# Kernel tuning notes

Hardware: AMD Instinct MI355X
Metric: run time of the kernel (lower is better)

## Reference

```python
import jax, jax.numpy as jnp
import numpy as np

EPS = 1e-5
N_NODES = 100000
N_EDGES = 1600000
IN_F, HID_F, OUT_F = 128, 128, 64


def setup_inputs() -> dict:
    key = jax.random.key(0)
    ks = jax.random.split(key, 8)
    def xavier(k, fan_in, fan_out):
        lim = float(np.sqrt(6.0 / (fan_in + fan_out)))
        return jax.random.uniform(k, (fan_in, fan_out), jnp.float32, -lim, lim)
    return {
        "features": jax.random.normal(ks[0], (N_NODES, IN_F), jnp.float32),
        "src": jax.random.randint(ks[1], (N_EDGES,), 0, N_NODES, jnp.int64 if jax.config.jax_enable_x64 else jnp.int32),
        "dst": jax.random.randint(ks[2], (N_EDGES,), 0, N_NODES, jnp.int64 if jax.config.jax_enable_x64 else jnp.int32),
        "W_self1": xavier(ks[3], IN_F, HID_F),
        "W_neigh1": xavier(ks[4], IN_F, HID_F),
        "b1": jnp.zeros((HID_F,), jnp.float32),
        "gamma1": jnp.ones((HID_F,), jnp.float32),
        "beta1": jnp.zeros((HID_F,), jnp.float32),
        "W_self2": xavier(ks[5], HID_F, OUT_F),
        "W_neigh2": xavier(ks[6], HID_F, OUT_F),
        "b2": jnp.zeros((OUT_F,), jnp.float32),
        "gamma2": jnp.ones((OUT_F,), jnp.float32),
        "beta2": jnp.zeros((OUT_F,), jnp.float32),
    }


def _sage_conv(h, src, dst, W_self, W_neigh, b, n_nodes):
    # mean aggregation of source-node features onto destination nodes
    agg = jax.ops.segment_sum(h[src], dst, num_segments=n_nodes)   # [N, d]
    deg = jax.ops.segment_sum(jnp.ones_like(dst, dtype=h.dtype), dst, num_segments=n_nodes)
    h_neigh = agg / jnp.maximum(deg, 1.0)[:, None]                  # zero-degree -> 0
    return h @ W_self + h_neigh @ W_neigh + b


def _batchnorm(h, gamma, beta):
    # training-mode BatchNorm1d: batch stats over node dim, biased variance
    mu = jnp.mean(h, axis=0)
    var = jnp.mean(jnp.square(h - mu), axis=0)
    return (h - mu) * jax.lax.rsqrt(var + EPS) * gamma + beta


def reference(features, src, dst, W_self1, W_neigh1, b1, gamma1, beta1,
              W_self2, W_neigh2, b2, gamma2, beta2):
    n = features.shape[0]
    h = _sage_conv(features, src, dst, W_self1, W_neigh1, b1, n)
    h = jax.nn.relu(_batchnorm(h, gamma1, beta1))
    h = _sage_conv(h, src, dst, W_self2, W_neigh2, b2, n)
    return _batchnorm(h, gamma2, beta2)
```

## Files before the change

### kernel.cpp

```cpp
#include <hip/hip_runtime.h>

#define EPS_BN 1e-5f
#define BINSHIFT 9
#define BINW 512
#define P_EPB 8192
#define LDS_CAP 10240
#define NREP 32

typedef __attribute__((ext_vector_type(8))) short short8;
typedef __attribute__((ext_vector_type(4))) float f32x4;

__device__ __forceinline__ unsigned short f2bf(float x) {
    unsigned int u = __float_as_uint(x);
    u += 0x7fffu + ((u >> 16) & 1u);
    return (unsigned short)(u >> 16);
}
__device__ __forceinline__ float bf2f(unsigned short h) {
    return __uint_as_float(((unsigned int)h) << 16);
}
__device__ __forceinline__ float bflo(unsigned u) { return __uint_as_float(u << 16); }
__device__ __forceinline__ float bfhi(unsigned u) { return __uint_as_float(u & 0xffff0000u); }

__device__ __forceinline__ void scan512(int* a, int t) {
    for (int off = 1; off < 512; off <<= 1) {
        int v = (t >= off) ? a[t - off] : 0;
        __syncthreads();
        a[t] += v;
        __syncthreads();
    }
}
__device__ __forceinline__ void scan256(int* a, int t) {
    for (int off = 1; off < 256; off <<= 1) {
        int v = (t >= off) ? a[t - off] : 0;
        __syncthreads();
        a[t] += v;
        __syncthreads();
    }
}

__global__ __launch_bounds__(256) void prep_kernel(
    const float* __restrict__ Ws1, const float* __restrict__ Wn1,
    const float* __restrict__ Ws2, const float* __restrict__ Wn2,
    unsigned short* __restrict__ W1f, unsigned short* __restrict__ W2f,
    const int* __restrict__ dst, int* __restrict__ counts, int E, int NB, int wB) {
    int tid = threadIdx.x;
    if (blockIdx.x < wB) {
        int i = blockIdx.x * 256 + tid;
        if (i < 128 * 256) {
            int j = i & 7, L = (i >> 3) & 63, c = (i >> 9) & 15, kk = i >> 13;
            int k = kk * 32 + (L >> 4) * 8 + j;
            int col = c * 16 + (L & 15);
            float v = (col < 128) ? Ws1[k * 128 + col] : Wn1[k * 128 + (col - 128)];
            W1f[i] = f2bf(v);
        } else {
            int idx = i - 128 * 256;
            if (idx < 128 * 128) {
                int j = idx & 7, L = (idx >> 3) & 63, c = (idx >> 9) & 7, kk = idx >> 12;
                int k = kk * 32 + (L >> 4) * 8 + j;
                int col = c * 16 + (L & 15);
                float v = (col < 64) ? Ws2[k * 64 + col] : Wn2[k * 64 + (col - 64)];
                W2f[idx] = f2bf(v);
            }
        }
    } else {
        __shared__ int hist[512];
        int blk = blockIdx.x - wB;
        int e0 = blk * P_EPB, e1 = min(e0 + P_EPB, E);
        for (int b = tid; b < 512; b += 256) hist[b] = 0;
        __syncthreads();
        for (int e = e0 + tid; e < e1; e += 256) atomicAdd(&hist[dst[e] >> BINSHIFT], 1);
        __syncthreads();
        for (int b = tid; b < NB; b += 256) counts[blk * NB + b] = hist[b];
    }
}

__global__ __launch_bounds__(256) void p2a(const int* __restrict__ counts,
                                           int* __restrict__ segrel,
                                           int* __restrict__ tot, int NB, int NBLK) {
    __shared__ int s[256];
    int b = blockIdx.x, t = threadIdx.x;
    int v = (t < NBLK) ? counts[t * NB + b] : 0;
    s[t] = v;
    __syncthreads();
    scan256(s, t);
    if (t < NBLK) segrel[t * NB + b] = s[t] - v;
    if (t == 255) tot[b] = s[255];
}

__global__ __launch_bounds__(512) void p3_scatter(const int* __restrict__ src,
                                                  const int* __restrict__ dst,
                                                  const int* __restrict__ segrel,
                                                  const int* __restrict__ tot,
                                                  unsigned* __restrict__ epack,
                                                  int E, int NB) {
    __shared__ unsigned lp[P_EPB];
    __shared__ int hist[512];
    __shared__ int sBase[513];
    __shared__ int cursor[512];
    __shared__ int bbase[512];
    int t = threadIdx.x;
    int blk = blockIdx.x;
    int e0 = blk * P_EPB, e1 = min(e0 + P_EPB, E), m = e1 - e0;
    int tv = (t < NB) ? tot[t] : 0;
    bbase[t] = tv;
    __syncthreads();
    scan512(bbase, t);
    bbase[t] -= tv;
    hist[t] = 0;
    __syncthreads();
    for (int e = e0 + t; e < e1; e += 512) atomicAdd(&hist[dst[e] >> BINSHIFT], 1);
    __syncthreads();
    int h = hist[t];
    scan512(hist, t);
    int excl = hist[t] - h;
    sBase[t] = excl;
    cursor[t] = excl;
    if (t == 0) sBase[512] = m;
    __syncthreads();
    for (int e = e0 + t; e < e1; e += 512) {
        int d = dst[e];
        int pos = atomicAdd(&cursor[d >> BINSHIFT], 1);
        lp[pos] = ((unsigned)src[e] << BINSHIFT) | ((unsigned)d & (BINW - 1));
    }
    __syncthreads();
    for (int i = t; i < m; i += 512) {
        int lo = 0, hi = NB;
        while (hi - lo > 1) {
            int mid = (lo + hi) >> 1;
            if (sBase[mid] <= i) lo = mid; else hi = mid;
        }
        epack[bbase[lo] + segrel[blk * NB + lo] + (i - sBase[lo])] = lp[i];
    }
}

__global__ __launch_bounds__(512) void p4_csr(const unsigned* __restrict__ epack,
                                              const int* __restrict__ tot,
                                              int* __restrict__ row_start,
                                              int* __restrict__ cntg,
                                              float* __restrict__ inv_deg,
                                              int* __restrict__ csr_src, int N, int NB) {
    __shared__ int ncnt[512];
    __shared__ int cursor[512];
    __shared__ int bb[512];
    __shared__ int lsrc[LDS_CAP];
    int t = threadIdx.x;
    int b = blockIdx.x;
    int tv = (t < NB) ? tot[t] : 0;
    bb[t] = tv;
    __syncthreads();
    scan512(bb, t);
    int e1 = bb[b];
    int e0 = bb[b] - tot[b];
    int m = e1 - e0;
    int nbase = b << BINSHIFT;
    int nn = min(N - nbase, BINW);
    ncnt[t] = 0;
    __syncthreads();
    for (int i = e0 + t; i < e1; i += 512)
        atomicAdd(&ncnt[epack[i] & (BINW - 1)], 1);
    __syncthreads();
    int c = ncnt[t];
    scan512(ncnt, t);
    int excl = ncnt[t] - c;
    if (t < nn) {
        int node = nbase + t;
        row_start[node] = e0 + excl;
        cntg[node] = c;
        inv_deg[node] = 1.0f / fmaxf((float)c, 1.0f);
    }
    cursor[t] = excl;
    __syncthreads();
    for (int i = e0 + t; i < e1; i += 512) {
        unsigned v = epack[i];
        int pos = atomicAdd(&cursor[v & (BINW - 1)], 1);
        if (pos < LDS_CAP) lsrc[pos] = (int)(v >> BINSHIFT);
    }
    __syncthreads();
    int mm = min(m, LDS_CAP);
    for (int i = t; i < mm; i += 512) csr_src[e0 + i] = lsrc[i];
}

template <int MT, int MSELF, bool SELFBF, bool FUSEBN, bool AFP32>
__global__ __launch_bounds__(256) void gemm_dual(const unsigned short* __restrict__ Ab,
                                                 const float* __restrict__ Af,
                                                 const unsigned short* __restrict__ Wf,
                                                 float* __restrict__ YselfF,
                                                 unsigned short* __restrict__ YselfB,
                                                 unsigned short* __restrict__ Ynb, int N,
                                                 const float* __restrict__ sums,
                                                 const float* __restrict__ gamma,
                                                 const float* __restrict__ beta,
                                                 float invN) {
    constexpr int K = 128;
    constexpr int NCT = MT / 16;
    constexpr int KS = K / 32;
    constexpr int MNB = MT - MSELF;
    __shared__ unsigned short Bl[KS * NCT * 64 * 8];
    __shared__ float ssc[128], ssh[128];

    for (int i = threadIdx.x; i < KS * NCT * 64; i += 256)
        ((short8*)Bl)[i] = ((const short8*)Wf)[i];
    if (FUSEBN && threadIdx.x < 128) {
        int c = threadIdx.x;
        float su = 0.f, sq = 0.f;
        for (int r = 0; r < NREP; r++) {
            su += sums[r * 256 + c];
            sq += sums[r * 256 + 128 + c];
        }
        float mu = su * invN;
        float var = sq * invN - mu * mu;
        float sc = gamma[c] * rsqrtf(var + EPS_BN);
        ssc[c] = sc;
        ssh[c] = beta[c] - mu * sc;
    }
    __syncthreads();

    int wv = threadIdx.x >> 6, lane = threadIdx.x & 63;
    int row0 = blockIdx.x * 128 + wv * 32;
    int m = lane & 15, quad = lane >> 4;

    short8 afrag[2][KS];
#pragma unroll
    for (int t = 0; t < 2; t++) {
        int arow = row0 + t * 16 + m;
        if (arow >= N) arow = N - 1;
#pragma unroll
        for (int kk = 0; kk < KS; kk++) {
            short8 raw;
            if (AFP32) {
                const float* ap = Af + (size_t)arow * K + quad * 8 + kk * 32;
                f32x4 a = *(const f32x4*)ap;
                f32x4 b = *(const f32x4*)(ap + 4);
#pragma unroll
                for (int j = 0; j < 4; j++) {
                    raw[j] = (short)f2bf(a[j]);
                    raw[4 + j] = (short)f2bf(b[j]);
                }
            } else {
                raw = *(const short8*)(Ab + (size_t)arow * K + quad * 8 + kk * 32);
            }
            if (FUSEBN) {
#pragma unroll
                for (int j = 0; j < 8; j++) {
                    int c = kk * 32 + quad * 8 + j;
                    float f = bf2f((unsigned short)raw[j]) * ssc[c] + ssh[c];
                    raw[j] = (short)f2bf(fmaxf(f, 0.f));
                }
            }
            afrag[t][kk] = raw;
        }
    }

    f32x4 acc[2][NCT];
#pragma unroll
    for (int t = 0; t < 2; t++)
        for (int c = 0; c < NCT; c++)
            for (int j = 0; j < 4; j++) acc[t][c][j] = 0.f;

#pragma unroll
    for (int kk = 0; kk < KS; kk++) {
#pragma unroll
        for (int c = 0; c < NCT; c++) {
            short8 bfrag = *(const short8*)&Bl[((kk * NCT + c) * 64 + lane) * 8];
#pragma unroll
            for (int t = 0; t < 2; t++)
                acc[t][c] = __builtin_amdgcn_mfma_f32_16x16x32_bf16(afrag[t][kk], bfrag,
                                                                    acc[t][c], 0, 0, 0);
        }
    }

#pragma unroll
    for (int t = 0; t < 2; t++) {
#pragma unroll
        for (int c = 0; c < NCT; c++) {
            int colg = c * 16 + m;
#pragma unroll
            for (int r = 0; r < 4; r++) {
                int row = row0 + t * 16 + quad * 4 + r;
                if (row < N) {
                    float v = acc[t][c][r];
                    if (colg < MSELF) {
                        if (SELFBF)
                            YselfB[(size_t)row * MSELF + colg] = f2bf(v);
                        else
                            YselfF[(size_t)row * MSELF + colg] = v;
                    } else {
                        Ynb[(size_t)row * MNB + (colg - MSELF)] = f2bf(v);
                    }
                }
            }
        }
    }
}

__global__ __launch_bounds__(256) void agg_row128(const unsigned int* __restrict__ Sb,
                                                  const unsigned int* __restrict__ T,
                                                  const int* __restrict__ row_start,
                                                  const int* __restrict__ cnt,
                                                  const float* __restrict__ inv_deg,
                                                  const int* __restrict__ csr_src,
                                                  const float* __restrict__ bias,
                                                  unsigned int* __restrict__ Out,
                                                  float* __restrict__ sums,
                                                  int N, int totalWaves) {
    int wv = threadIdx.x >> 6, lane = threadIdx.x & 63;
    int c = lane * 2;
    float bs0 = bias[c], bs1 = bias[c + 1];
    float S0 = 0.f, S1 = 0.f, Q0 = 0.f, Q1 = 0.f;
    for (int n = blockIdx.x * 4 + wv; n < N; n += totalWaves) {
        int start = row_start[n];
        int ec = cnt[n];
        float inv = inv_deg[n];
        float a0 = 0.f, a1 = 0.f;
        int e = 0;
        for (; e + 7 < ec; e += 8) {
            int i0 = csr_src[start + e];
            int i1 = csr_src[start + e + 1];
            int i2 = csr_src[start + e + 2];
            int i3 = csr_src[start + e + 3];
            int i4 = csr_src[start + e + 4];
            int i5 = csr_src[start + e + 5];
            int i6 = csr_src[start + e + 6];
            int i7 = csr_src[start + e + 7];
            unsigned u0 = T[(size_t)i0 * 64 + lane];
            unsigned u1 = T[(size_t)i1 * 64 + lane];
            unsigned u2 = T[(size_t)i2 * 64 + lane];
            unsigned u3 = T[(size_t)i3 * 64 + lane];
            unsigned u4 = T[(size_t)i4 * 64 + lane];
            unsigned u5 = T[(size_t)i5 * 64 + lane];
            unsigned u6 = T[(size_t)i6 * 64 + lane];
            unsigned u7 = T[(size_t)i7 * 64 + lane];
            a0 += bflo(u0) + bflo(u1) + bflo(u2) + bflo(u3) +
                  bflo(u4) + bflo(u5) + bflo(u6) + bflo(u7);
            a1 += bfhi(u0) + bfhi(u1) + bfhi(u2) + bfhi(u3) +
                  bfhi(u4) + bfhi(u5) + bfhi(u6) + bfhi(u7);
        }
        for (; e < ec; e++) {
            unsigned u0 = T[(size_t)csr_src[start + e] * 64 + lane];
            a0 += bflo(u0);
            a1 += bfhi(u0);
        }
        unsigned su = Sb[(size_t)n * 64 + lane];
        float h0 = bflo(su) + a0 * inv + bs0;
        float h1 = bfhi(su) + a1 * inv + bs1;
        Out[(size_t)n * 64 + lane] = (unsigned)f2bf(h0) | ((unsigned)f2bf(h1) << 16);
        S0 += h0; Q0 += h0 * h0;
        S1 += h1; Q1 += h1 * h1;
    }
    __shared__ float ls[256];
    ls[threadIdx.x] = 0.f;
    __syncthreads();
    atomicAdd(&ls[c], S0);
    atomicAdd(&ls[c + 1], S1);
    atomicAdd(&ls[128 + c], Q0);
    atomicAdd(&ls[129 + c], Q1);
    __syncthreads();
    float* dstS = sums + (size_t)(blockIdx.x & (NREP - 1)) * 256;
    atomicAdd(&dstS[threadIdx.x], ls[threadIdx.x]);
}

__global__ __launch_bounds__(256) void agg_row64(const unsigned int* __restrict__ T,
                                                 const int* __restrict__ row_start,
                                                 const int* __restrict__ cnt,
                                                 const float* __restrict__ inv_deg,
                                                 const int* __restrict__ csr_src,
                                                 const float* __restrict__ bias,
                                                 float* Self, float* __restrict__ sums,
                                                 int N, int totalHalf) {
    int wv = threadIdx.x >> 6, L = threadIdx.x & 63;
    int g = L >> 5, h = L & 31;
    int c = h * 2;
    float bs0 = bias[c], bs1 = bias[c + 1];
    float S0 = 0.f, S1 = 0.f, Q0 = 0.f, Q1 = 0.f;
    for (int n = (blockIdx.x * 4 + wv) * 2 + g; n < N; n += totalHalf) {
        int start = row_start[n];
        int ec = cnt[n];
        float inv = inv_deg[n];
        float a0 = 0.f, a1 = 0.f;
        int e = 0;
        for (; e + 3 < ec; e += 4) {
            int i0 = csr_src[start + e];
            int i1 = csr_src[start + e + 1];
            int i2 = csr_src[start + e + 2];
            int i3 = csr_src[start + e + 3];
            unsigned u0 = T[(size_t)i0 * 32 + h];
            unsigned u1 = T[(size_t)i1 * 32 + h];
            unsigned u2 = T[(size_t)i2 * 32 + h];
            unsigned u3 = T[(size_t)i3 * 32 + h];
            a0 += bflo(u0) + bflo(u1) + bflo(u2) + bflo(u3);
            a1 += bfhi(u0) + bfhi(u1) + bfhi(u2) + bfhi(u3);
        }
        for (; e < ec; e++) {
            unsigned u0 = T[(size_t)csr_src[start + e] * 32 + h];
            a0 += bflo(u0);
            a1 += bfhi(u0);
        }
        size_t off = (size_t)n * 64 + c;
        float h0 = Self[off] + a0 * inv + bs0;
        float h1 = Self[off + 1] + a1 * inv + bs1;
        Self[off] = h0;
        Self[off + 1] = h1;
        S0 += h0; Q0 += h0 * h0;
        S1 += h1; Q1 += h1 * h1;
    }
    __shared__ float ls[128];
    if (threadIdx.x < 128) ls[threadIdx.x] = 0.f;
    __syncthreads();
    atomicAdd(&ls[c], S0);
    atomicAdd(&ls[c + 1], S1);
    atomicAdd(&ls[64 + c], Q0);
    atomicAdd(&ls[65 + c], Q1);
    __syncthreads();
    if (threadIdx.x < 128) {
        float* dstS = sums + (size_t)(blockIdx.x & (NREP - 1)) * 128;
        atomicAdd(&dstS[threadIdx.x], ls[threadIdx.x]);
    }
}

__global__ __launch_bounds__(256) void bn_apply_f64(float* H, const float* __restrict__ sums,
                                                    const float* __restrict__ gamma,
                                                    const float* __restrict__ beta,
                                                    int N, float invN) {
    __shared__ float ss[128];
    int tid = threadIdx.x;
    if (tid < 64) {
        float su = 0.f, sq = 0.f;
        for (int r = 0; r < NREP; r++) {
            su += sums[r * 128 + tid];
            sq += sums[r * 128 + 64 + tid];
        }
        float mu = su * invN;
        float var = sq * invN - mu * mu;
        float sc = gamma[tid] * rsqrtf(var + EPS_BN);
        ss[tid] = sc;
        ss[64 + tid] = beta[tid] - mu * sc;
    }
    __syncthreads();
    int total4 = N * 16;
    float4* H4 = (float4*)H;
    for (int i = blockIdx.x * 256 + threadIdx.x; i < total4; i += 256 * gridDim.x) {
        int c0 = (i * 4) & 63;
        float4 v = H4[i];
        float4 sc = *(const float4*)&ss[c0];
        float4 sh = *(const float4*)&ss[64 + c0];
        v.x = v.x * sc.x + sh.x;
        v.y = v.y * sc.y + sh.y;
        v.z = v.z * sc.z + sh.z;
        v.w = v.w * sc.w + sh.w;
        H4[i] = v;
    }
}

extern "C" void kernel_launch(void* const* d_in, const int* in_sizes, int n_in,
                              void* d_out, int out_size, void* d_ws, size_t ws_size,
                              hipStream_t stream) {
    const float* X = (const float*)d_in[0];
    const int* src = (const int*)d_in[1];
    const int* dst = (const int*)d_in[2];
    const float* Wself1 = (const float*)d_in[3];
    const float* Wneigh1 = (const float*)d_in[4];
    const float* b1 = (const float*)d_in[5];
    const float* g1 = (const float*)d_in[6];
    const float* be1 = (const float*)d_in[7];
    const float* Wself2 = (const float*)d_in[8];
    const float* Wneigh2 = (const float*)d_in[9];
    const float* b2 = (const float*)d_in[10];
    const float* g2 = (const float*)d_in[11];
    const float* be2 = (const float*)d_in[12];
    float* out = (float*)d_out;

    const int N = in_sizes[0] / 128;
    const int E = in_sizes[1];
    const int NB = (N + BINW - 1) >> BINSHIFT;
    const int NBLK = (E + P_EPB - 1) / P_EPB;

    char* p = (char*)d_ws;
    auto carve = [&](size_t bytes) {
        char* r = p;
        p += (bytes + 255) & ~(size_t)255;
        return r;
    };
    float* sums1 = (float*)carve((size_t)NREP * 256 * 4);
    float* sums2 = (float*)carve((size_t)NREP * 128 * 4);
    size_t zero_bytes = (size_t)(p - (char*)d_ws);
    int* counts = (int*)carve((size_t)NBLK * NB * 4);
    int* segrel = (int*)carve((size_t)NBLK * NB * 4);
    int* tot = (int*)carve((size_t)NB * 4);
    unsigned* epack = (unsigned*)carve((size_t)E * 4);
    int* csr_src = (int*)carve((size_t)E * 4);
    int* row_start = (int*)carve((size_t)N * 4);
    int* cntg = (int*)carve((size_t)N * 4);
    float* inv_deg = (float*)carve((size_t)N * 4);
    unsigned short* W1f = (unsigned short*)carve(128 * 256 * 2);
    unsigned short* W2f = (unsigned short*)carve(128 * 128 * 2);
    unsigned short* bufS = (unsigned short*)carve((size_t)N * 128 * 2);
    unsigned short* tab = (unsigned short*)carve((size_t)N * 128 * 2);
    unsigned short* h1b = (unsigned short*)carve((size_t)N * 128 * 2);

    hipMemsetAsync(d_ws, 0, zero_bytes, stream);

    const int wB = 192;
    const float invN = 1.0f / (float)N;
    prep_kernel<<<wB + NBLK, 256, 0, stream>>>(Wself1, Wneigh1, Wself2, Wneigh2, W1f, W2f,
                                               dst, counts, E, NB, wB);
    p2a<<<NB, 256, 0, stream>>>(counts, segrel, tot, NB, NBLK);
    p3_scatter<<<NBLK, 512, 0, stream>>>(src, dst, segrel, tot, epack, E, NB);
    p4_csr<<<NB, 512, 0, stream>>>(epack, tot, row_start, cntg, inv_deg, csr_src, N, NB);

    int ggrid = (N + 127) / 128;
    gemm_dual<256, 128, true, false, true><<<ggrid, 256, 0, stream>>>(
        nullptr, X, W1f, nullptr, bufS, tab, N, nullptr, nullptr, nullptr, 0.f);
    agg_row128<<<2048, 256, 0, stream>>>(
        (const unsigned int*)bufS, (const unsigned int*)tab, row_start, cntg, inv_deg,
        csr_src, b1, (unsigned int*)h1b, sums1, N, 8192);

    gemm_dual<128, 64, false, true, false><<<ggrid, 256, 0, stream>>>(
        h1b, nullptr, W2f, out, nullptr, tab, N, sums1, g1, be1, invN);
    agg_row64<<<2048, 256, 0, stream>>>(
        (const unsigned int*)tab, row_start, cntg, inv_deg, csr_src, b2, out, sums2,
        N, 16384);
    bn_apply_f64<<<2048, 256, 0, stream>>>(out, sums2, g2, be2, N, invN);
}
```

Measured before the change: 353.9 us.

## Merge histogram with first GEMM, drop scan kernel, fold weight prep into GEMMs

Fuses the per-block dst histogram with the layer-1 dual GEMM into one launch, so the two independent jobs share a grid. It removes the separate p2a scan kernel by having p3_scatter and p4_csr recompute per-bin totals and prefix offsets directly from the counts array. It drops the weight-prep kernel by converting fp32 weights to the swizzled bf16 layout inside each GEMM block, at the cost of redundant conversion work per block. The gather loops in both aggregation kernels are unrolled deeper to keep more loads in flight.

```diff
diff --git a/kernel.cpp b/kernel.cpp
--- a/kernel.cpp
+++ b/kernel.cpp
@@ -29,179 +29,36 @@
         __syncthreads();
     }
 }
-__device__ __forceinline__ void scan256(int* a, int t) {
-    for (int off = 1; off < 256; off <<= 1) {
-        int v = (t >= off) ? a[t - off] : 0;
-        __syncthreads();
-        a[t] += v;
-        __syncthreads();
-    }
-}
-
-__global__ __launch_bounds__(256) void prep_kernel(
-    const float* __restrict__ Ws1, const float* __restrict__ Wn1,
-    const float* __restrict__ Ws2, const float* __restrict__ Wn2,
-    unsigned short* __restrict__ W1f, unsigned short* __restrict__ W2f,
-    const int* __restrict__ dst, int* __restrict__ counts, int E, int NB, int wB) {
-    int tid = threadIdx.x;
-    if (blockIdx.x < wB) {
-        int i = blockIdx.x * 256 + tid;
-        if (i < 128 * 256) {
-            int j = i & 7, L = (i >> 3) & 63, c = (i >> 9) & 15, kk = i >> 13;
-            int k = kk * 32 + (L >> 4) * 8 + j;
-            int col = c * 16 + (L & 15);
-            float v = (col < 128) ? Ws1[k * 128 + col] : Wn1[k * 128 + (col - 128)];
-            W1f[i] = f2bf(v);
-        } else {
-            int idx = i - 128 * 256;
-            if (idx < 128 * 128) {
-                int j = idx & 7, L = (idx >> 3) & 63, c = (idx >> 9) & 7, kk = idx >> 12;
-                int k = kk * 32 + (L >> 4) * 8 + j;
-                int col = c * 16 + (L & 15);
-                float v = (col < 64) ? Ws2[k * 64 + col] : Wn2[k * 64 + (col - 64)];
-                W2f[idx] = f2bf(v);
-            }
-        }
-    } else {
-        __shared__ int hist[512];
-        int blk = blockIdx.x - wB;
-        int e0 = blk * P_EPB, e1 = min(e0 + P_EPB, E);
-        for (int b = tid; b < 512; b += 256) hist[b] = 0;
-        __syncthreads();
-        for (int e = e0 + tid; e < e1; e += 256) atomicAdd(&hist[dst[e] >> BINSHIFT], 1);
-        __syncthreads();
-        for (int b = tid; b < NB; b += 256) counts[blk * NB + b] = hist[b];
-    }
-}
-
-__global__ __launch_bounds__(256) void p2a(const int* __restrict__ counts,
-                                           int* __restrict__ segrel,
-                                           int* __restrict__ tot, int NB, int NBLK) {
-    __shared__ int s[256];
-    int b = blockIdx.x, t = threadIdx.x;
-    int v = (t < NBLK) ? counts[t * NB + b] : 0;
-    s[t] = v;
-    __syncthreads();
-    scan256(s, t);
-    if (t < NBLK) segrel[t * NB + b] = s[t] - v;
-    if (t == 255) tot[b] = s[255];
-}
-
-__global__ __launch_bounds__(512) void p3_scatter(const int* __restrict__ src,
-                                                  const int* __restrict__ dst,
-                                                  const int* __restrict__ segrel,
-                                                  const int* __restrict__ tot,
-                                                  unsigned* __restrict__ epack,
-                                                  int E, int NB) {
-    __shared__ unsigned lp[P_EPB];
-    __shared__ int hist[512];
-    __shared__ int sBase[513];
-    __shared__ int cursor[512];
-    __shared__ int bbase[512];
-    int t = threadIdx.x;
-    int blk = blockIdx.x;
-    int e0 = blk * P_EPB, e1 = min(e0 + P_EPB, E), m = e1 - e0;
-    int tv = (t < NB) ? tot[t] : 0;
-    bbase[t] = tv;
-    __syncthreads();
-    scan512(bbase, t);
-    bbase[t] -= tv;
-    hist[t] = 0;
-    __syncthreads();
-    for (int e = e0 + t; e < e1; e += 512) atomicAdd(&hist[dst[e] >> BINSHIFT], 1);
-    __syncthreads();
-    int h = hist[t];
-    scan512(hist, t);
-    int excl = hist[t] - h;
-    sBase[t] = excl;
-    cursor[t] = excl;
-    if (t == 0) sBase[512] = m;
-    __syncthreads();
-    for (int e = e0 + t; e < e1; e += 512) {
-        int d = dst[e];
-        int pos = atomicAdd(&cursor[d >> BINSHIFT], 1);
-        lp[pos] = ((unsigned)src[e] << BINSHIFT) | ((unsigned)d & (BINW - 1));
-    }
-    __syncthreads();
-    for (int i = t; i < m; i += 512) {
-        int lo = 0, hi = NB;
-        while (hi - lo > 1) {
-            int mid = (lo + hi) >> 1;
-            if (sBase[mid] <= i) lo = mid; else hi = mid;
-        }
-        epack[bbase[lo] + segrel[blk * NB + lo] + (i - sBase[lo])] = lp[i];
-    }
-}
-
-__global__ __launch_bounds__(512) void p4_csr(const unsigned* __restrict__ epack,
-                                              const int* __restrict__ tot,
-                                              int* __restrict__ row_start,
-                                              int* __restrict__ cntg,
-                                              float* __restrict__ inv_deg,
-                                              int* __restrict__ csr_src, int N, int NB) {
-    __shared__ int ncnt[512];
-    __shared__ int cursor[512];
-    __shared__ int bb[512];
-    __shared__ int lsrc[LDS_CAP];
-    int t = threadIdx.x;
-    int b = blockIdx.x;
-    int tv = (t < NB) ? tot[t] : 0;
-    bb[t] = tv;
-    __syncthreads();
-    scan512(bb, t);
-    int e1 = bb[b];
-    int e0 = bb[b] - tot[b];
-    int m = e1 - e0;
-    int nbase = b << BINSHIFT;
-    int nn = min(N - nbase, BINW);
-    ncnt[t] = 0;
-    __syncthreads();
-    for (int i = e0 + t; i < e1; i += 512)
-        atomicAdd(&ncnt[epack[i] & (BINW - 1)], 1);
-    __syncthreads();
-    int c = ncnt[t];
-    scan512(ncnt, t);
-    int excl = ncnt[t] - c;
-    if (t < nn) {
-        int node = nbase + t;
-        row_start[node] = e0 + excl;
-        cntg[node] = c;
-        inv_deg[node] = 1.0f / fmaxf((float)c, 1.0f);
-    }
-    cursor[t] = excl;
-    __syncthreads();
-    for (int i = e0 + t; i < e1; i += 512) {
-        unsigned v = epack[i];
-        int pos = atomicAdd(&cursor[v & (BINW - 1)], 1);
-        if (pos < LDS_CAP) lsrc[pos] = (int)(v >> BINSHIFT);
-    }
-    __syncthreads();
-    int mm = min(m, LDS_CAP);
-    for (int i = t; i < mm; i += 512) csr_src[e0 + i] = lsrc[i];
-}
 
 template <int MT, int MSELF, bool SELFBF, bool FUSEBN, bool AFP32>
-__global__ __launch_bounds__(256) void gemm_dual(const unsigned short* __restrict__ Ab,
-                                                 const float* __restrict__ Af,
-                                                 const unsigned short* __restrict__ Wf,
-                                                 float* __restrict__ YselfF,
-                                                 unsigned short* __restrict__ YselfB,
-                                                 unsigned short* __restrict__ Ynb, int N,
-                                                 const float* __restrict__ sums,
-                                                 const float* __restrict__ gamma,
-                                                 const float* __restrict__ beta,
-                                                 float invN) {
+__device__ __forceinline__ void gemm_body(int bid, const unsigned short* __restrict__ Ab,
+                                          const float* __restrict__ Af,
+                                          const float* __restrict__ Ws,
+                                          const float* __restrict__ Wn,
+                                          float* __restrict__ YselfF,
+                                          unsigned short* __restrict__ YselfB,
+                                          unsigned short* __restrict__ Ynb, int N,
+                                          const float* __restrict__ sums,
+                                          const float* __restrict__ gamma,
+                                          const float* __restrict__ beta, float invN) {
     constexpr int K = 128;
     constexpr int NCT = MT / 16;
     constexpr int KS = K / 32;
     constexpr int MNB = MT - MSELF;
+    constexpr int CL = (NCT == 16) ? 4 : 3;
     __shared__ unsigned short Bl[KS * NCT * 64 * 8];
     __shared__ float ssc[128], ssh[128];
-
-    for (int i = threadIdx.x; i < KS * NCT * 64; i += 256)
-        ((short8*)Bl)[i] = ((const short8*)Wf)[i];
-    if (FUSEBN && threadIdx.x < 128) {
-        int c = threadIdx.x;
+    int tid = threadIdx.x;
+
+    for (int i = tid; i < KS * NCT * 64 * 8; i += 256) {
+        int j = i & 7, L = (i >> 3) & 63, c = (i >> 9) & (NCT - 1), kk = i >> (9 + CL);
+        int k = kk * 32 + (L >> 4) * 8 + j;
+        int col = c * 16 + (L & 15);
+        float v = (col < MSELF) ? Ws[k * MSELF + col] : Wn[k * MNB + (col - MSELF)];
+        Bl[i] = f2bf(v);
+    }
+    if (FUSEBN && tid < 128) {
+        int c = tid;
         float su = 0.f, sq = 0.f;
         for (int r = 0; r < NREP; r++) {
             su += sums[r * 256 + c];
@@ -215,8 +72,8 @@
     }
     __syncthreads();
 
-    int wv = threadIdx.x >> 6, lane = threadIdx.x & 63;
-    int row0 = blockIdx.x * 128 + wv * 32;
+    int wv = tid >> 6, lane = tid & 63;
+    int row0 = bid * 128 + wv * 32;
     int m = lane & 15, quad = lane >> 4;
 
     short8 afrag[2][KS];
@@ -291,6 +148,145 @@
             }
         }
     }
+}
+
+__global__ __launch_bounds__(256) void k1_front(const int* __restrict__ dst,
+                                                int* __restrict__ counts, int E, int NB,
+                                                int NBLK, const float* __restrict__ X,
+                                                const float* __restrict__ Ws1,
+                                                const float* __restrict__ Wn1,
+                                                unsigned short* __restrict__ bufS,
+                                                unsigned short* __restrict__ tab, int N) {
+    if ((int)blockIdx.x < NBLK) {
+        __shared__ int hist[512];
+        int tid = threadIdx.x;
+        int blk = blockIdx.x;
+        int e0 = blk * P_EPB, e1 = min(e0 + P_EPB, E);
+        for (int b = tid; b < 512; b += 256) hist[b] = 0;
+        __syncthreads();
+        for (int e = e0 + tid; e < e1; e += 256) atomicAdd(&hist[dst[e] >> BINSHIFT], 1);
+        __syncthreads();
+        for (int b = tid; b < NB; b += 256) counts[blk * NB + b] = hist[b];
+    } else {
+        gemm_body<256, 128, true, false, true>(blockIdx.x - NBLK, nullptr, X, Ws1, Wn1,
+                                               nullptr, bufS, tab, N, nullptr, nullptr,
+                                               nullptr, 0.f);
+    }
+}
+
+__global__ __launch_bounds__(256) void gemm2_kernel(const unsigned short* __restrict__ h1b,
+                                                    const float* __restrict__ Ws2,
+                                                    const float* __restrict__ Wn2,
+                                                    float* __restrict__ out,
+                                                    unsigned short* __restrict__ tab, int N,
+                                                    const float* __restrict__ sums,
+                                                    const float* __restrict__ g1,
+                                                    const float* __restrict__ be1,
+                                                    float invN) {
+    gemm_body<128, 64, false, true, false>(blockIdx.x, h1b, nullptr, Ws2, Wn2, out,
+                                           nullptr, tab, N, sums, g1, be1, invN);
+}
+
+__global__ __launch_bounds__(512) void p3_scatter(const int* __restrict__ src,
+                                                  const int* __restrict__ dst,
+                                                  const int* __restrict__ counts,
+                                                  unsigned* __restrict__ epack,
+                                                  int E, int NB, int NBLK) {
+    __shared__ unsigned lp[P_EPB];
+    __shared__ int hist[512];
+    __shared__ int sBase[513];
+    __shared__ int cursor[512];
+    __shared__ int bexcl[512];
+    __shared__ int myrel[512];
+    int t = threadIdx.x;
+    int blk = blockIdx.x;
+    int e0 = blk * P_EPB, e1 = min(e0 + P_EPB, E), m = e1 - e0;
+    int cs = 0, ms = 0;
+    if (t < NB)
+        for (int q = 0; q < NBLK; q++) {
+            int v = counts[q * NB + t];
+            cs += v;
+            if (q < blk) ms += v;
+        }
+    myrel[t] = ms;
+    bexcl[t] = cs;
+    __syncthreads();
+    scan512(bexcl, t);
+    bexcl[t] -= cs;
+    hist[t] = 0;
+    __syncthreads();
+    for (int e = e0 + t; e < e1; e += 512) atomicAdd(&hist[dst[e] >> BINSHIFT], 1);
+    __syncthreads();
+    int h = hist[t];
+    scan512(hist, t);
+    int excl = hist[t] - h;
+    sBase[t] = excl;
+    cursor[t] = excl;
+    if (t == 0) sBase[512] = m;
+    __syncthreads();
+    for (int e = e0 + t; e < e1; e += 512) {
+        int d = dst[e];
+        int pos = atomicAdd(&cursor[d >> BINSHIFT], 1);
+        lp[pos] = ((unsigned)src[e] << BINSHIFT) | ((unsigned)d & (BINW - 1));
+    }
+    __syncthreads();
+    for (int i = t; i < m; i += 512) {
+        int lo = 0, hi = NB;
+        while (hi - lo > 1) {
+            int mid = (lo + hi) >> 1;
+            if (sBase[mid] <= i) lo = mid; else hi = mid;
+        }
+        epack[bexcl[lo] + myrel[lo] + (i - sBase[lo])] = lp[i];
+    }
+}
+
+__global__ __launch_bounds__(512) void p4_csr(const unsigned* __restrict__ epack,
+                                              const int* __restrict__ counts,
+                                              int* __restrict__ row_start,
+                                              int* __restrict__ cntg,
+                                              float* __restrict__ inv_deg,
+                                              int* __restrict__ csr_src, int N, int NB,
+                                              int NBLK) {
+    __shared__ int ncnt[512];
+    __shared__ int cursor[512];
+    __shared__ int bb[512];
+    __shared__ int lsrc[LDS_CAP];
+    int t = threadIdx.x;
+    int b = blockIdx.x;
+    int cs = 0;
+    if (t < NB)
+        for (int q = 0; q < NBLK; q++) cs += counts[q * NB + t];
+    bb[t] = cs;
+    __syncthreads();
+    scan512(bb, t);
+    int e1 = bb[b];
+    int e0 = (b > 0) ? bb[b - 1] : 0;
+    int m = e1 - e0;
+    int nbase = b << BINSHIFT;
+    int nn = min(N - nbase, BINW);
+    ncnt[t] = 0;
+    __syncthreads();
+    for (int i = e0 + t; i < e1; i += 512) atomicAdd(&ncnt[epack[i] & (BINW - 1)], 1);
+    __syncthreads();
+    int c = ncnt[t];
+    scan512(ncnt, t);
+    int excl = ncnt[t] - c;
+    if (t < nn) {
+        int node = nbase + t;
+        row_start[node] = e0 + excl;
+        cntg[node] = c;
+        inv_deg[node] = 1.0f / fmaxf((float)c, 1.0f);
+    }
+    cursor[t] = excl;
+    __syncthreads();
+    for (int i = e0 + t; i < e1; i += 512) {
+        unsigned v = epack[i];
+        int pos = atomicAdd(&cursor[v & (BINW - 1)], 1);
+        if (pos < LDS_CAP) lsrc[pos] = (int)(v >> BINSHIFT);
+    }
+    __syncthreads();
+    int mm = min(m, LDS_CAP);
+    for (int i = t; i < mm; i += 512) csr_src[e0 + i] = lsrc[i];
 }
 
 __global__ __launch_bounds__(256) void agg_row128(const unsigned int* __restrict__ Sb,
@@ -313,27 +309,31 @@
         float inv = inv_deg[n];
         float a0 = 0.f, a1 = 0.f;
         int e = 0;
-        for (; e + 7 < ec; e += 8) {
-            int i0 = csr_src[start + e];
-            int i1 = csr_src[start + e + 1];
-            int i2 = csr_src[start + e + 2];
-            int i3 = csr_src[start + e + 3];
-            int i4 = csr_src[start + e + 4];
-            int i5 = csr_src[start + e + 5];
-            int i6 = csr_src[start + e + 6];
-            int i7 = csr_src[start + e + 7];
-            unsigned u0 = T[(size_t)i0 * 64 + lane];
-            unsigned u1 = T[(size_t)i1 * 64 + lane];
-            unsigned u2 = T[(size_t)i2 * 64 + lane];
-            unsigned u3 = T[(size_t)i3 * 64 + lane];
-            unsigned u4 = T[(size_t)i4 * 64 + lane];
-            unsigned u5 = T[(size_t)i5 * 64 + lane];
-            unsigned u6 = T[(size_t)i6 * 64 + lane];
-            unsigned u7 = T[(size_t)i7 * 64 + lane];
-            a0 += bflo(u0) + bflo(u1) + bflo(u2) + bflo(u3) +
-                  bflo(u4) + bflo(u5) + bflo(u6) + bflo(u7);
-            a1 += bfhi(u0) + bfhi(u1) + bfhi(u2) + bfhi(u3) +
-                  bfhi(u4) + bfhi(u5) + bfhi(u6) + bfhi(u7);
+        for (; e + 15 < ec; e += 16) {
+            int idx[16];
+            unsigned uu[16];
+#pragma unroll
+            for (int q = 0; q < 16; q++) idx[q] = csr_src[start + e + q];
+#pragma unroll
+            for (int q = 0; q < 16; q++) uu[q] = T[(size_t)idx[q] * 64 + lane];
+#pragma unroll
+            for (int q = 0; q < 16; q++) {
+                a0 += bflo(uu[q]);
+                a1 += bfhi(uu[q]);
+            }
+        }
+        for (; e + 3 < ec; e += 4) {
+            int idx[4];
+            unsigned uu[4];
+#pragma unroll
+            for (int q = 0; q < 4; q++) idx[q] = csr_src[start + e + q];
+#pragma unroll
+            for (int q = 0; q < 4; q++) uu[q] = T[(size_t)idx[q] * 64 + lane];
+#pragma unroll
+            for (int q = 0; q < 4; q++) {
+                a0 += bflo(uu[q]);
+                a1 += bfhi(uu[q]);
+            }
         }
         for (; e < ec; e++) {
             unsigned u0 = T[(size_t)csr_src[start + e] * 64 + lane];
@@ -378,17 +378,18 @@
         float inv = inv_deg[n];
         float a0 = 0.f, a1 = 0.f;
         int e = 0;
-        for (; e + 3 < ec; e += 4) {
-            int i0 = csr_src[start + e];
-            int i1 = csr_src[start + e + 1];
-            int i2 = csr_src[start + e + 2];
-            int i3 = csr_src[start + e + 3];
-            unsigned u0 = T[(size_t)i0 * 32 + h];
-            unsigned u1 = T[(size_t)i1 * 32 + h];
-            unsigned u2 = T[(size_t)i2 * 32 + h];
-            unsigned u3 = T[(size_t)i3 * 32 + h];
-            a0 += bflo(u0) + bflo(u1) + bflo(u2) + bflo(u3);
-            a1 += bfhi(u0) + bfhi(u1) + bfhi(u2) + bfhi(u3);
+        for (; e + 7 < ec; e += 8) {
+            int idx[8];
+            unsigned uu[8];
+#pragma unroll
+            for (int q = 0; q < 8; q++) idx[q] = csr_src[start + e + q];
+#pragma unroll
+            for (int q = 0; q < 8; q++) uu[q] = T[(size_t)idx[q] * 32 + h];
+#pragma unroll
+            for (int q = 0; q < 8; q++) {
+                a0 += bflo(uu[q]);
+                a1 += bfhi(uu[q]);
+            }
         }
         for (; e < ec; e++) {
             unsigned u0 = T[(size_t)csr_src[start + e] * 32 + h];
@@ -484,38 +485,30 @@
     float* sums2 = (float*)carve((size_t)NREP * 128 * 4);
     size_t zero_bytes = (size_t)(p - (char*)d_ws);
     int* counts = (int*)carve((size_t)NBLK * NB * 4);
-    int* segrel = (int*)carve((size_t)NBLK * NB * 4);
-    int* tot = (int*)carve((size_t)NB * 4);
     unsigned* epack = (unsigned*)carve((size_t)E * 4);
     int* csr_src = (int*)carve((size_t)E * 4);
     int* row_start = (int*)carve((size_t)N * 4);
     int* cntg = (int*)carve((size_t)N * 4);
     float* inv_deg = (float*)carve((size_t)N * 4);
-    unsigned short* W1f = (unsigned short*)carve(128 * 256 * 2);
-    unsigned short* W2f = (unsigned short*)carve(128 * 128 * 2);
     unsigned short* bufS = (unsigned short*)carve((size_t)N * 128 * 2);
     unsigned short* tab = (unsigned short*)carve((size_t)N * 128 * 2);
     unsigned short* h1b = (unsigned short*)carve((size_t)N * 128 * 2);
 
     hipMemsetAsync(d_ws, 0, zero_bytes, stream);
 
-    const int wB = 192;
     const float invN = 1.0f / (float)N;
-    prep_kernel<<<wB + NBLK, 256, 0, stream>>>(Wself1, Wneigh1, Wself2, Wneigh2, W1f, W2f,
-                                               dst, counts, E, NB, wB);
-    p2a<<<NB, 256, 0, stream>>>(counts, segrel, tot, NB, NBLK);
-    p3_scatter<<<NBLK, 512, 0, stream>>>(src, dst, segrel, tot, epack, E, NB);
-    p4_csr<<<NB, 512, 0, stream>>>(epack, tot, row_start, cntg, inv_deg, csr_src, N, NB);
-
-    int ggrid = (N + 127) / 128;
-    gemm_dual<256, 128, true, false, true><<<ggrid, 256, 0, stream>>>(
-        nullptr, X, W1f, nullptr, bufS, tab, N, nullptr, nullptr, nullptr, 0.f);
+    const int ggrid = (N + 127) / 128;
+
+    k1_front<<<NBLK + ggrid, 256, 0, stream>>>(dst, counts, E, NB, NBLK, X, Wself1,
+                                               Wneigh1, bufS, tab, N);
+    p3_scatter<<<NBLK, 512, 0, stream>>>(src, dst, counts, epack, E, NB, NBLK);
+    p4_csr<<<NB, 512, 0, stream>>>(epack, counts, row_start, cntg, inv_deg, csr_src, N,
+                                   NB, NBLK);
     agg_row128<<<2048, 256, 0, stream>>>(
         (const unsigned int*)bufS, (const unsigned int*)tab, row_start, cntg, inv_deg,
         csr_src, b1, (unsigned int*)h1b, sums1, N, 8192);
-
-    gemm_dual<128, 64, false, true, false><<<ggrid, 256, 0, stream>>>(
-        h1b, nullptr, W2f, out, nullptr, tab, N, sums1, g1, be1, invN);
+    gemm2_kernel<<<ggrid, 256, 0, stream>>>(h1b, Wself2, Wneigh2, out, tab, N, sums1, g1,
+                                            be1, invN);
     agg_row64<<<2048, 256, 0, stream>>>(
         (const unsigned int*)tab, row_start, cntg, inv_deg, csr_src, b2, out, sums2,
         N, 16384);
```

New measurement: 467.0 us. +32.0%, slower.
